# Kernel optimization log

Hardware: AMD Instinct MI355X
Metric: run time of the kernel (lower is better)

Reference implementation:

```python
import jax, jax.numpy as jnp
import numpy as np

N, E, B = 50000, 1600000, 64
VOCAB, EMB = 1000, 16
HID, OUT_FEAT = 192, 128   # hidden_sf*model_dim, out_sf*output_channels
MODEL_DIM, DEMO, OUT_DIM = 64, 5, 2
EPS = 1e-7  # GENConv eps


def setup_inputs() -> dict:
    key = jax.random.key(0)
    ks = jax.random.split(key, 18)
    f32 = jnp.float32

    def rn(k, shape, scale):
        return jax.random.normal(k, shape, dtype=f32) * scale

    node_idx = jax.random.randint(ks[0], (N,), 0, VOCAB)
    edge_index = jax.random.randint(ks[1], (2, E), 0, N)
    batch = jnp.sort(jax.random.randint(ks[2], (N,), 0, B))
    demographics = rn(ks[3], (B, DEMO), 1.0)

    emb = rn(ks[4], (VOCAB, EMB), 1.0)
    dims = [(EMB, HID), (HID, HID), (HID, HID), (HID, OUT_FEAT)]
    params = {}
    for i, (din, dout) in enumerate(dims):
        params[f"W{i}"] = rn(ks[5 + 2 * i], (din, dout), 1.0 / np.sqrt(din))
        params[f"b{i}"] = jnp.zeros((dout,), f32)
    params["Wc1"] = rn(ks[13], (OUT_FEAT + DEMO, MODEL_DIM), 1.0 / np.sqrt(OUT_FEAT + DEMO))
    params["bc1"] = jnp.zeros((MODEL_DIM,), f32)
    params["Wc2"] = rn(ks[14], (MODEL_DIM, OUT_DIM), 1.0 / np.sqrt(MODEL_DIM))
    params["bc2"] = jnp.zeros((OUT_DIM,), f32)

    return {"node_idx": node_idx, "edge_index": edge_index, "batch": batch,
            "demographics": demographics, "emb": emb, **params}


def _gen_conv(x, src, dst, W, b):
    # GENConv (num_layers=1, aggr='add', edge_attr=None):
    #   out_i = Linear( sum_{j->i} (relu(x_j) + eps) + x_i )
    m = jax.nn.relu(x) + EPS                                   # [N, D]
    agg = jax.ops.segment_sum(m[src], dst, num_segments=x.shape[0])
    return (agg + x) @ W + b


def reference(node_idx, edge_index, batch, demographics, emb,
              W0, b0, W1, b1, W2, b2, W3, b3, Wc1, bc1, Wc2, bc2):
    x = emb[node_idx]                                          # [N, 16]
    src, dst = edge_index[0], edge_index[1]
    for W, b in ((W0, b0), (W1, b1), (W2, b2), (W3, b3)):
        x = _gen_conv(x, src, dst, W, b)                       # [N, D_l]
    # global_mean_pool
    cnt = jax.ops.segment_sum(jnp.ones((x.shape[0],), x.dtype), batch, num_segments=B)
    g = jax.ops.segment_sum(x, batch, num_segments=B) / jnp.maximum(cnt, 1.0)[:, None]
    feats = jnp.concatenate([g, demographics], axis=1)         # [B, 133]
    h = jax.nn.relu(feats @ Wc1 + bc1)                         # dropout = identity (eval)
    return h @ Wc2 + bc2                                       # [B, out_dim]
```

## Files before the change

### kernel.cpp

```cpp
#include <hip/hip_runtime.h>
#include <stdint.h>

#define EPS 1e-7f

constexpr int N_NODES = 50000;
constexpr int N_EDGES = 1600000;
constexpr int BATCH = 64;
constexpr int EMB = 16;
constexpr int HID = 192;
constexpr int OUTF = 128;
constexpr int DEMO = 5;
constexpr int MODEL_DIM = 64;
constexpr int OUT_DIM = 2;

constexpr int NPART = 8;
constexpr int PART_NODES = (N_NODES + NPART - 1) / NPART;

constexpr int SCAN_CHUNK = 256;
constexpr int NCHUNK = (N_NODES + SCAN_CHUNK - 1) / SCAN_CHUNK;

typedef unsigned short bf16_t;
typedef short s8v __attribute__((ext_vector_type(8)));
typedef float f4v __attribute__((ext_vector_type(4)));

static __device__ __forceinline__ float bf2f(bf16_t u) {
  return __uint_as_float(((uint32_t)u) << 16);
}
static __device__ __forceinline__ bf16_t f2bf(float f) {
  uint32_t b = __float_as_uint(f);
  return (bf16_t)((b + 0x7FFFu + ((b >> 16) & 1u)) >> 16);
}

__global__ void emb_gather(const int* __restrict__ idx, const float* __restrict__ emb,
                           bf16_t* __restrict__ x) {
  int t = blockIdx.x * blockDim.x + threadIdx.x;
  if (t >= N_NODES * EMB) return;
  int node = t / EMB, f = t % EMB;
  x[t] = f2bf(emb[idx[node] * EMB + f]);
}

__global__ void hist_kernel(const int* __restrict__ dst, int* __restrict__ deg) {
  int part = blockIdx.x & (NPART - 1);
  int blk = blockIdx.x >> 3;
  int nthread = (gridDim.x >> 3) * blockDim.x;
  int lo = part * PART_NODES, hi = lo + PART_NODES;
  for (int e = blk * blockDim.x + threadIdx.x; e < N_EDGES; e += nthread) {
    int d = dst[e];
    if (d >= lo && d < hi) atomicAdd(&deg[d], 1);
  }
}

__global__ void chunk_sum_kernel(const int* __restrict__ deg, int* __restrict__ chunk_sum) {
  int i = blockIdx.x * SCAN_CHUNK + threadIdx.x;
  int v = (i < N_NODES) ? deg[i] : 0;
#pragma unroll
  for (int off = 32; off > 0; off >>= 1) v += __shfl_down(v, off);
  __shared__ int s[SCAN_CHUNK / 64];
  if ((threadIdx.x & 63) == 0) s[threadIdx.x >> 6] = v;
  __syncthreads();
  if (threadIdx.x == 0) {
    int t = 0;
#pragma unroll
    for (int w = 0; w < SCAN_CHUNK / 64; ++w) t += s[w];
    chunk_sum[blockIdx.x] = t;
  }
}

__global__ void scan_chunks_kernel(const int* __restrict__ chunk_sum,
                                   int* __restrict__ chunk_off) {
  __shared__ int s[256];
  int t = threadIdx.x;
  int v = (t < NCHUNK) ? chunk_sum[t] : 0;
  s[t] = v;
  __syncthreads();
  for (int off = 1; off < 256; off <<= 1) {
    int u = (t >= off) ? s[t - off] : 0;
    __syncthreads();
    s[t] += u;
    __syncthreads();
  }
  if (t < NCHUNK) chunk_off[t] = s[t] - v;
}

__global__ void chunk_scan_write_kernel(const int* __restrict__ deg,
                                        const int* __restrict__ chunk_off,
                                        int* __restrict__ row_start,
                                        int* __restrict__ cursor) {
  __shared__ int s[SCAN_CHUNK];
  int t = threadIdx.x;
  int i = blockIdx.x * SCAN_CHUNK + t;
  int v = (i < N_NODES) ? deg[i] : 0;
  s[t] = v;
  __syncthreads();
  for (int off = 1; off < SCAN_CHUNK; off <<= 1) {
    int u = (t >= off) ? s[t - off] : 0;
    __syncthreads();
    s[t] += u;
    __syncthreads();
  }
  int excl = chunk_off[blockIdx.x] + s[t] - v;
  if (i < N_NODES) {
    row_start[i] = excl;
    cursor[i] = excl;
    if (i == N_NODES - 1) row_start[N_NODES] = excl + v;
  }
}

__global__ void scatter_kernel(const int* __restrict__ src, const int* __restrict__ dst,
                               int* __restrict__ cursor, int* __restrict__ csr_src) {
  int part = blockIdx.x & (NPART - 1);
  int blk = blockIdx.x >> 3;
  int nthread = (gridDim.x >> 3) * blockDim.x;
  int lo = part * PART_NODES, hi = lo + PART_NODES;
  for (int e = blk * blockDim.x + threadIdx.x; e < N_EDGES; e += nthread) {
    int d = dst[e];
    if (d >= lo && d < hi) {
      int pos = atomicAdd(&cursor[d], 1);
      csr_src[pos] = src[e];
    }
  }
}

template <int TPN, int NPB>
__global__ void agg2_kernel(const uint32_t* __restrict__ x, const int* __restrict__ row_start,
                            const int* __restrict__ csr_src, uint32_t* __restrict__ out) {
  int f = threadIdx.x % TPN;
  int node = blockIdx.x * NPB + threadIdx.x / TPN;
  if (node >= N_NODES) return;
  int s0 = row_start[node], s1 = row_start[node + 1];
  float deps = (float)(s1 - s0) * EPS;
  uint32_t xv = x[(size_t)node * TPN + f];
  float a0 = __uint_as_float(xv << 16) + deps;
  float a1 = __uint_as_float(xv & 0xFFFF0000u) + deps;
  int e = s0;
  for (; e + 8 <= s1; e += 8) {
    int idx[8];
#pragma unroll
    for (int j = 0; j < 8; ++j) idx[j] = csr_src[e + j];
    uint32_t v[8];
#pragma unroll
    for (int j = 0; j < 8; ++j) v[j] = x[(size_t)idx[j] * TPN + f];
#pragma unroll
    for (int j = 0; j < 8; ++j) {
      a0 += fmaxf(__uint_as_float(v[j] << 16), 0.f);
      a1 += fmaxf(__uint_as_float(v[j] & 0xFFFF0000u), 0.f);
    }
  }
  for (; e < s1; ++e) {
    uint32_t v = x[(size_t)csr_src[e] * TPN + f];
    a0 += fmaxf(__uint_as_float(v << 16), 0.f);
    a1 += fmaxf(__uint_as_float(v & 0xFFFF0000u), 0.f);
  }
  out[(size_t)node * TPN + f] = (uint32_t)f2bf(a0) | ((uint32_t)f2bf(a1) << 16);
}

__global__ void wprep_kernel(const float* __restrict__ W, int K, int NOUT,
                             bf16_t* __restrict__ Wt) {
  int t = blockIdx.x * blockDim.x + threadIdx.x;
  if (t >= K * NOUT) return;
  int k = t / NOUT, n = t % NOUT;
  Wt[(size_t)n * K + k] = f2bf(W[t]);
}

template <int NOUT, bool OUT_BF16>
__global__ void mfma_gemm(const bf16_t* __restrict__ in, const bf16_t* __restrict__ Wt,
                          const float* __restrict__ bias, void* __restrict__ outp) {
  constexpr int K = 192;
  constexpr int KT = K / 32;
  constexpr int NT = NOUT / 16;
  int wave = threadIdx.x >> 6;
  int lane = threadIdx.x & 63;
  int tile = blockIdx.x * 4 + wave;
  if (tile >= N_NODES / 16) return;

  int rlo = lane & 15;
  int kbase = (lane >> 4) * 8;

  s8v a[KT];
  const bf16_t* ap = in + ((size_t)(tile * 16 + rlo)) * K + kbase;
#pragma unroll
  for (int kt = 0; kt < KT; ++kt) a[kt] = *(const s8v*)(ap + kt * 32);

  int r0 = (lane >> 4) * 4;
#pragma unroll
  for (int nt = 0; nt < NT; ++nt) {
    const bf16_t* wp = Wt + ((size_t)(nt * 16 + rlo)) * K + kbase;
    f4v c = {0.f, 0.f, 0.f, 0.f};
#pragma unroll
    for (int kt = 0; kt < KT; ++kt) {
      s8v b = *(const s8v*)(wp + kt * 32);
      c = __builtin_amdgcn_mfma_f32_16x16x32_bf16(a[kt], b, c, 0, 0, 0);
    }
    float bv = bias[nt * 16 + rlo];
#pragma unroll
    for (int r = 0; r < 4; ++r) {
      float v = c[r] + bv;
      size_t o = (size_t)(tile * 16 + r0 + r) * NOUT + nt * 16 + rlo;
      if constexpr (OUT_BF16) ((bf16_t*)outp)[o] = f2bf(v);
      else                    ((float*)outp)[o] = v;
    }
  }
}

template <int DIN, int DOUT, bool OUT_BF16>
__global__ void gemm_kernel(const bf16_t* __restrict__ in, const float* __restrict__ W,
                            const float* __restrict__ bias, void* __restrict__ outp) {
  constexpr int ROWS = 16;
  __shared__ bf16_t tile[ROWS * DIN];
  int c = threadIdx.x;
  int base = blockIdx.x * ROWS;

  {
    const uint4* gsrc = reinterpret_cast<const uint4*>(in + (size_t)base * DIN);
    uint4* ldst = reinterpret_cast<uint4*>(tile);
    constexpr int NV = ROWS * DIN * 2 / 16;
    for (int i = threadIdx.x; i < NV; i += blockDim.x) ldst[i] = gsrc[i];
  }
  __syncthreads();

  float acc[ROWS];
  float bc = bias[c];
#pragma unroll
  for (int r = 0; r < ROWS; ++r) acc[r] = bc;

  for (int k0 = 0; k0 < DIN; k0 += 8) {
    float w[8];
#pragma unroll
    for (int j = 0; j < 8; ++j) w[j] = W[(size_t)(k0 + j) * DOUT + c];
#pragma unroll
    for (int r = 0; r < ROWS; ++r) {
      uint4 packed = *reinterpret_cast<const uint4*>(&tile[r * DIN + k0]);
      uint32_t pk[4] = {packed.x, packed.y, packed.z, packed.w};
#pragma unroll
      for (int q = 0; q < 4; ++q) {
        float lo = __uint_as_float(pk[q] << 16);
        float hi = __uint_as_float(pk[q] & 0xFFFF0000u);
        acc[r] = fmaf(lo, w[2 * q], acc[r]);
        acc[r] = fmaf(hi, w[2 * q + 1], acc[r]);
      }
    }
  }

#pragma unroll
  for (int r = 0; r < ROWS; ++r) {
    size_t o = (size_t)(base + r) * DOUT + c;
    if constexpr (OUT_BF16) ((bf16_t*)outp)[o] = f2bf(acc[r]);
    else                    ((float*)outp)[o] = acc[r];
  }
}

constexpr int POOL_CHUNK = 100;
__global__ void pool_kernel(const float* __restrict__ x, const int* __restrict__ batch,
                            float* __restrict__ gsum, int* __restrict__ gcnt) {
  int f = threadIdx.x;
  int start = blockIdx.x * POOL_CHUNK;
  if (start >= N_NODES) return;
  int end = min(start + POOL_CHUNK, N_NODES);
  int cur = batch[start];
  float acc = 0.f;
  int cnt = 0;
  for (int i = start; i < end; ++i) {
    int b = batch[i];
    if (b != cur) {
      atomicAdd(&gsum[cur * OUTF + f], acc);
      if (f == 0) atomicAdd(&gcnt[cur], cnt);
      acc = 0.f; cnt = 0; cur = b;
    }
    acc += x[(size_t)i * OUTF + f];
    cnt++;
  }
  atomicAdd(&gsum[cur * OUTF + f], acc);
  if (f == 0) atomicAdd(&gcnt[cur], cnt);
}

__global__ void mlp_kernel(const float* __restrict__ gsum, const int* __restrict__ gcnt,
                           const float* __restrict__ demo,
                           const float* __restrict__ Wc1, const float* __restrict__ bc1,
                           const float* __restrict__ Wc2, const float* __restrict__ bc2,
                           float* __restrict__ out) {
  int b = blockIdx.x;
  int c = threadIdx.x;
  __shared__ float feats[OUTF + DEMO];
  float inv = 1.f / fmaxf((float)gcnt[b], 1.f);
  for (int k = c; k < OUTF; k += MODEL_DIM) feats[k] = gsum[b * OUTF + k] * inv;
  if (c < DEMO) feats[OUTF + c] = demo[b * DEMO + c];
  __syncthreads();
  float s = bc1[c];
#pragma unroll
  for (int k = 0; k < OUTF + DEMO; ++k) s = fmaf(feats[k], Wc1[k * MODEL_DIM + c], s);
  float h = fmaxf(s, 0.f);
  float o0 = h * Wc2[c * OUT_DIM + 0];
  float o1 = h * Wc2[c * OUT_DIM + 1];
#pragma unroll
  for (int off = 32; off > 0; off >>= 1) {
    o0 += __shfl_down(o0, off);
    o1 += __shfl_down(o1, off);
  }
  if (c == 0) {
    out[b * OUT_DIM + 0] = o0 + bc2[0];
    out[b * OUT_DIM + 1] = o1 + bc2[1];
  }
}

extern "C" void kernel_launch(void* const* d_in, const int* in_sizes, int n_in,
                              void* d_out, int out_size, void* d_ws, size_t ws_size,
                              hipStream_t stream) {
  const int*   node_idx = (const int*)d_in[0];
  const int*   edge_index = (const int*)d_in[1];
  const int*   batch = (const int*)d_in[2];
  const float* demo = (const float*)d_in[3];
  const float* emb  = (const float*)d_in[4];
  const float* W0 = (const float*)d_in[5];  const float* b0 = (const float*)d_in[6];
  const float* W1 = (const float*)d_in[7];  const float* b1 = (const float*)d_in[8];
  const float* W2 = (const float*)d_in[9];  const float* b2 = (const float*)d_in[10];
  const float* W3 = (const float*)d_in[11]; const float* b3 = (const float*)d_in[12];
  const float* Wc1 = (const float*)d_in[13]; const float* bc1 = (const float*)d_in[14];
  const float* Wc2 = (const float*)d_in[15]; const float* bc2 = (const float*)d_in[16];
  const int* src = edge_index;
  const int* dst = edge_index + N_EDGES;
  float* out = (float*)d_out;

  char* ws = (char*)d_ws;
  size_t off = 0;
  auto alloc = [&](size_t bytes) {
    void* p = ws + off;
    off += (bytes + 255) & ~size_t(255);
    return p;
  };
  bf16_t* xbf     = (bf16_t*)alloc((size_t)N_NODES * HID * 2);
  bf16_t* aggbf   = (bf16_t*)alloc((size_t)N_NODES * HID * 2);
  float*  x3      = (float*)alloc((size_t)N_NODES * OUTF * 4);
  int*   csr_src  = (int*)alloc((size_t)N_EDGES * 4);
  int*   deg      = (int*)alloc((size_t)N_NODES * 4);
  int*   row_start= (int*)alloc((size_t)(N_NODES + 1) * 4);
  int*   cursor   = (int*)alloc((size_t)N_NODES * 4);
  int*   chunk_sum= (int*)alloc((size_t)NCHUNK * 4);
  int*   chunk_off= (int*)alloc((size_t)NCHUNK * 4);
  float* gsum     = (float*)alloc((size_t)BATCH * OUTF * 4);
  int*   gcnt     = (int*)alloc((size_t)BATCH * 4);
  bf16_t* Wt1     = (bf16_t*)alloc((size_t)HID * HID * 2);
  bf16_t* Wt2     = (bf16_t*)alloc((size_t)HID * HID * 2);
  bf16_t* Wt3     = (bf16_t*)alloc((size_t)OUTF * HID * 2);

  hipMemsetAsync(deg, 0, (size_t)N_NODES * 4, stream);
  hipMemsetAsync(gsum, 0, (size_t)BATCH * OUTF * 4, stream);
  hipMemsetAsync(gcnt, 0, (size_t)BATCH * 4, stream);

  wprep_kernel<<<(HID * HID + 255) / 256, 256, 0, stream>>>(W1, HID, HID, Wt1);
  wprep_kernel<<<(HID * HID + 255) / 256, 256, 0, stream>>>(W2, HID, HID, Wt2);
  wprep_kernel<<<(HID * OUTF + 255) / 256, 256, 0, stream>>>(W3, HID, OUTF, Wt3);

  hist_kernel<<<NPART * 256, 256, 0, stream>>>(dst, deg);
  chunk_sum_kernel<<<NCHUNK, SCAN_CHUNK, 0, stream>>>(deg, chunk_sum);
  scan_chunks_kernel<<<1, 256, 0, stream>>>(chunk_sum, chunk_off);
  chunk_scan_write_kernel<<<NCHUNK, SCAN_CHUNK, 0, stream>>>(deg, chunk_off, row_start, cursor);
  scatter_kernel<<<NPART * 256, 256, 0, stream>>>(src, dst, cursor, csr_src);

  constexpr int TILES = N_NODES / 16;
  constexpr int GBLK = (TILES + 3) / 4;

  emb_gather<<<(N_NODES * EMB + 255) / 256, 256, 0, stream>>>(node_idx, emb, xbf);
  agg2_kernel<8, 32><<<(N_NODES + 31) / 32, 256, 0, stream>>>(
      (const uint32_t*)xbf, row_start, csr_src, (uint32_t*)aggbf);
  gemm_kernel<16, 192, true><<<N_NODES / 16, 192, 0, stream>>>(aggbf, W0, b0, xbf);
  agg2_kernel<96, 2><<<(N_NODES + 1) / 2, 192, 0, stream>>>(
      (const uint32_t*)xbf, row_start, csr_src, (uint32_t*)aggbf);
  mfma_gemm<192, true><<<GBLK, 256, 0, stream>>>(aggbf, Wt1, b1, xbf);
  agg2_kernel<96, 2><<<(N_NODES + 1) / 2, 192, 0, stream>>>(
      (const uint32_t*)xbf, row_start, csr_src, (uint32_t*)aggbf);
  mfma_gemm<192, true><<<GBLK, 256, 0, stream>>>(aggbf, Wt2, b2, xbf);
  agg2_kernel<96, 2><<<(N_NODES + 1) / 2, 192, 0, stream>>>(
      (const uint32_t*)xbf, row_start, csr_src, (uint32_t*)aggbf);
  mfma_gemm<128, false><<<GBLK, 256, 0, stream>>>(aggbf, Wt3, b3, x3);

  pool_kernel<<<(N_NODES + POOL_CHUNK - 1) / POOL_CHUNK, OUTF, 0, stream>>>(x3, batch, gsum, gcnt);
  mlp_kernel<<<BATCH, MODEL_DIM, 0, stream>>>(gsum, gcnt, demo, Wc1, bc1, Wc2, bc2, out);
}
```

Measured before the change: 588.3 us.

## Split hidden-layer aggregation into feature-column slices across blocks

Replaces the per-node full-row gather aggregation for the 192-wide layers with a sliced kernel. Each block handles 16 nodes and only one eighth of the feature columns (12 packed bf16 pairs). Consecutive block IDs map to different slices, aiming to improve cache locality for the randomly gathered source rows, since each slice's working set is smaller. In exchange, neighbour indices are re-read once per slice and each gather touches only 48 bytes per row, which may lower memory coalescing efficiency.

```diff
diff --git a/kernel.cpp b/kernel.cpp
--- a/kernel.cpp
+++ b/kernel.cpp
@@ -152,6 +152,47 @@
     a1 += fmaxf(__uint_as_float(v & 0xFFFF0000u), 0.f);
   }
   out[(size_t)node * TPN + f] = (uint32_t)f2bf(a0) | ((uint32_t)f2bf(a1) << 16);
+}
+
+constexpr int SL_TPN = 12;
+constexpr int SL_NPB = 16;
+__global__ void agg2_slice_kernel(const uint32_t* __restrict__ x,
+                                  const int* __restrict__ row_start,
+                                  const int* __restrict__ csr_src,
+                                  uint32_t* __restrict__ out) {
+  constexpr int ROW = HID / 2;
+  int slice = blockIdx.x & (NPART - 1);
+  int grp = blockIdx.x >> 3;
+  int f = threadIdx.x % SL_TPN;
+  int node = grp * SL_NPB + threadIdx.x / SL_TPN;
+  if (node >= N_NODES) return;
+  int col = slice * SL_TPN + f;
+  int s0 = row_start[node], s1 = row_start[node + 1];
+  float deps = (float)(s1 - s0) * EPS;
+  const uint32_t* xc = x + col;
+  uint32_t xv = xc[(size_t)node * ROW];
+  float a0 = __uint_as_float(xv << 16) + deps;
+  float a1 = __uint_as_float(xv & 0xFFFF0000u) + deps;
+  int e = s0;
+  for (; e + 8 <= s1; e += 8) {
+    int idx[8];
+#pragma unroll
+    for (int j = 0; j < 8; ++j) idx[j] = csr_src[e + j];
+    uint32_t v[8];
+#pragma unroll
+    for (int j = 0; j < 8; ++j) v[j] = xc[(size_t)idx[j] * ROW];
+#pragma unroll
+    for (int j = 0; j < 8; ++j) {
+      a0 += fmaxf(__uint_as_float(v[j] << 16), 0.f);
+      a1 += fmaxf(__uint_as_float(v[j] & 0xFFFF0000u), 0.f);
+    }
+  }
+  for (; e < s1; ++e) {
+    uint32_t v = xc[(size_t)csr_src[e] * ROW];
+    a0 += fmaxf(__uint_as_float(v << 16), 0.f);
+    a1 += fmaxf(__uint_as_float(v & 0xFFFF0000u), 0.f);
+  }
+  out[(size_t)node * ROW + col] = (uint32_t)f2bf(a0) | ((uint32_t)f2bf(a1) << 16);
 }
 
 __global__ void wprep_kernel(const float* __restrict__ W, int K, int NOUT,
@@ -358,18 +399,19 @@
 
   constexpr int TILES = N_NODES / 16;
   constexpr int GBLK = (TILES + 3) / 4;
+  constexpr int SL_GRID = NPART * ((N_NODES + SL_NPB - 1) / SL_NPB);
 
   emb_gather<<<(N_NODES * EMB + 255) / 256, 256, 0, stream>>>(node_idx, emb, xbf);
   agg2_kernel<8, 32><<<(N_NODES + 31) / 32, 256, 0, stream>>>(
       (const uint32_t*)xbf, row_start, csr_src, (uint32_t*)aggbf);
   gemm_kernel<16, 192, true><<<N_NODES / 16, 192, 0, stream>>>(aggbf, W0, b0, xbf);
-  agg2_kernel<96, 2><<<(N_NODES + 1) / 2, 192, 0, stream>>>(
+  agg2_slice_kernel<<<SL_GRID, SL_TPN * SL_NPB, 0, stream>>>(
       (const uint32_t*)xbf, row_start, csr_src, (uint32_t*)aggbf);
   mfma_gemm<192, true><<<GBLK, 256, 0, stream>>>(aggbf, Wt1, b1, xbf);
-  agg2_kernel<96, 2><<<(N_NODES + 1) / 2, 192, 0, stream>>>(
+  agg2_slice_kernel<<<SL_GRID, SL_TPN * SL_NPB, 0, stream>>>(
       (const uint32_t*)xbf, row_start, csr_src, (uint32_t*)aggbf);
   mfma_gemm<192, true><<<GBLK, 256, 0, stream>>>(aggbf, Wt2, b2, xbf);
-  agg2_kernel<96, 2><<<(N_NODES + 1) / 2, 192, 0, stream>>>(
+  agg2_slice_kernel<<<SL_GRID, SL_TPN * SL_NPB, 0, stream>>>(
       (const uint32_t*)xbf, row_start, csr_src, (uint32_t*)aggbf);
   mfma_gemm<128, false><<<GBLK, 256, 0, stream>>>(aggbf, Wt3, b3, x3);
 
```

After: 1.121 ms. +90.6%, slower.

## Bucket CSR neighbors by source range and vectorize 192-wide aggregation

Applied to the files above, without the earlier changes.

CSR construction now counts edges per (destination, source bucket) pair, with 16 buckets, and scans that larger histogram. Within each row, neighbor indices end up grouped by source-node range, which is meant to improve L2 locality of the gathers during aggregation. The 192-wide aggregation layers also switch to a new kernel in which each thread loads 16-byte uint4 vectors (8 bf16 features), giving fewer, wider memory requests per neighbor. The cost is a 16x larger histogram with its memset, a longer scan, and more scattered atomics during CSR build.

```diff
diff --git a/kernel.cpp b/kernel.cpp
--- a/kernel.cpp
+++ b/kernel.cpp
@@ -16,8 +16,12 @@
 constexpr int NPART = 8;
 constexpr int PART_NODES = (N_NODES + NPART - 1) / NPART;
 
-constexpr int SCAN_CHUNK = 256;
-constexpr int NCHUNK = (N_NODES + SCAN_CHUNK - 1) / SCAN_CHUNK;
+constexpr int NBKT = 16;
+constexpr int BKT_DIV = (N_NODES + NBKT - 1) / NBKT;
+constexpr int NB2 = N_NODES * NBKT;
+
+constexpr int SCAN2_CHUNK = 1024;
+constexpr int NCHUNK2 = (NB2 + SCAN2_CHUNK - 1) / SCAN2_CHUNK;
 
 typedef unsigned short bf16_t;
 typedef short s8v __attribute__((ext_vector_type(8)));
@@ -39,39 +43,67 @@
   x[t] = f2bf(emb[idx[node] * EMB + f]);
 }
 
-__global__ void hist_kernel(const int* __restrict__ dst, int* __restrict__ deg) {
+__global__ void hist2_kernel(const int* __restrict__ src, const int* __restrict__ dst,
+                             int* __restrict__ hist2) {
   int part = blockIdx.x & (NPART - 1);
   int blk = blockIdx.x >> 3;
   int nthread = (gridDim.x >> 3) * blockDim.x;
   int lo = part * PART_NODES, hi = lo + PART_NODES;
   for (int e = blk * blockDim.x + threadIdx.x; e < N_EDGES; e += nthread) {
     int d = dst[e];
-    if (d >= lo && d < hi) atomicAdd(&deg[d], 1);
-  }
-}
-
-__global__ void chunk_sum_kernel(const int* __restrict__ deg, int* __restrict__ chunk_sum) {
-  int i = blockIdx.x * SCAN_CHUNK + threadIdx.x;
-  int v = (i < N_NODES) ? deg[i] : 0;
+    if (d >= lo && d < hi) atomicAdd(&hist2[d * NBKT + src[e] / BKT_DIV], 1);
+  }
+}
+
+__global__ void chunk_sum2_kernel(const int* __restrict__ hist2, int* __restrict__ chunk_sum) {
+  int t = threadIdx.x;
+  int base = blockIdx.x * SCAN2_CHUNK + t * 4;
+  int v = 0;
+#pragma unroll
+  for (int j = 0; j < 4; ++j) {
+    int i = base + j;
+    if (i < NB2) v += hist2[i];
+  }
 #pragma unroll
   for (int off = 32; off > 0; off >>= 1) v += __shfl_down(v, off);
-  __shared__ int s[SCAN_CHUNK / 64];
-  if ((threadIdx.x & 63) == 0) s[threadIdx.x >> 6] = v;
+  __shared__ int s[4];
+  if ((t & 63) == 0) s[t >> 6] = v;
   __syncthreads();
-  if (threadIdx.x == 0) {
-    int t = 0;
-#pragma unroll
-    for (int w = 0; w < SCAN_CHUNK / 64; ++w) t += s[w];
-    chunk_sum[blockIdx.x] = t;
-  }
-}
-
-__global__ void scan_chunks_kernel(const int* __restrict__ chunk_sum,
-                                   int* __restrict__ chunk_off) {
+  if (t == 0) chunk_sum[blockIdx.x] = s[0] + s[1] + s[2] + s[3];
+}
+
+__global__ void scan_chunks2_kernel(const int* __restrict__ chunk_sum,
+                                    int* __restrict__ chunk_off) {
+  __shared__ int s[1024];
+  int t = threadIdx.x;
+  int v = (t < NCHUNK2) ? chunk_sum[t] : 0;
+  s[t] = v;
+  __syncthreads();
+  for (int off = 1; off < 1024; off <<= 1) {
+    int u = (t >= off) ? s[t - off] : 0;
+    __syncthreads();
+    s[t] += u;
+    __syncthreads();
+  }
+  if (t < NCHUNK2) chunk_off[t] = s[t] - v;
+}
+
+__global__ void chunk_scan_write2_kernel(const int* __restrict__ hist2,
+                                         const int* __restrict__ chunk_off,
+                                         int* __restrict__ cursor2,
+                                         int* __restrict__ row_start) {
   __shared__ int s[256];
   int t = threadIdx.x;
-  int v = (t < NCHUNK) ? chunk_sum[t] : 0;
-  s[t] = v;
+  int base = blockIdx.x * SCAN2_CHUNK + t * 4;
+  int local[4];
+  int tsum = 0;
+#pragma unroll
+  for (int j = 0; j < 4; ++j) {
+    int i = base + j;
+    local[j] = (i < NB2) ? hist2[i] : 0;
+    tsum += local[j];
+  }
+  s[t] = tsum;
   __syncthreads();
   for (int off = 1; off < 256; off <<= 1) {
     int u = (t >= off) ? s[t - off] : 0;
@@ -79,35 +111,21 @@
     s[t] += u;
     __syncthreads();
   }
-  if (t < NCHUNK) chunk_off[t] = s[t] - v;
-}
-
-__global__ void chunk_scan_write_kernel(const int* __restrict__ deg,
-                                        const int* __restrict__ chunk_off,
-                                        int* __restrict__ row_start,
-                                        int* __restrict__ cursor) {
-  __shared__ int s[SCAN_CHUNK];
-  int t = threadIdx.x;
-  int i = blockIdx.x * SCAN_CHUNK + t;
-  int v = (i < N_NODES) ? deg[i] : 0;
-  s[t] = v;
-  __syncthreads();
-  for (int off = 1; off < SCAN_CHUNK; off <<= 1) {
-    int u = (t >= off) ? s[t - off] : 0;
-    __syncthreads();
-    s[t] += u;
-    __syncthreads();
-  }
-  int excl = chunk_off[blockIdx.x] + s[t] - v;
-  if (i < N_NODES) {
-    row_start[i] = excl;
-    cursor[i] = excl;
-    if (i == N_NODES - 1) row_start[N_NODES] = excl + v;
+  int run = chunk_off[blockIdx.x] + s[t] - tsum;
+#pragma unroll
+  for (int j = 0; j < 4; ++j) {
+    int i = base + j;
+    if (i < NB2) {
+      cursor2[i] = run;
+      if ((i & (NBKT - 1)) == 0) row_start[i / NBKT] = run;
+      if (i == NB2 - 1) row_start[N_NODES] = run + local[j];
+      run += local[j];
+    }
   }
 }
 
 __global__ void scatter_kernel(const int* __restrict__ src, const int* __restrict__ dst,
-                               int* __restrict__ cursor, int* __restrict__ csr_src) {
+                               int* __restrict__ cursor2, int* __restrict__ csr_src) {
   int part = blockIdx.x & (NPART - 1);
   int blk = blockIdx.x >> 3;
   int nthread = (gridDim.x >> 3) * blockDim.x;
@@ -115,8 +133,9 @@
   for (int e = blk * blockDim.x + threadIdx.x; e < N_EDGES; e += nthread) {
     int d = dst[e];
     if (d >= lo && d < hi) {
-      int pos = atomicAdd(&cursor[d], 1);
-      csr_src[pos] = src[e];
+      int s = src[e];
+      int pos = atomicAdd(&cursor2[d * NBKT + s / BKT_DIV], 1);
+      csr_src[pos] = s;
     }
   }
 }
@@ -152,6 +171,61 @@
     a1 += fmaxf(__uint_as_float(v & 0xFFFF0000u), 0.f);
   }
   out[(size_t)node * TPN + f] = (uint32_t)f2bf(a0) | ((uint32_t)f2bf(a1) << 16);
+}
+
+constexpr int A4_TPN = 24;
+constexpr int A4_NPB = 8;
+__global__ void agg4_kernel(const uint4* __restrict__ x, const int* __restrict__ row_start,
+                            const int* __restrict__ csr_src, uint4* __restrict__ out) {
+  constexpr int ROW = 24;
+  int f = threadIdx.x % A4_TPN;
+  int node = blockIdx.x * A4_NPB + threadIdx.x / A4_TPN;
+  if (node >= N_NODES) return;
+  int s0 = row_start[node], s1 = row_start[node + 1];
+  float deps = (float)(s1 - s0) * EPS;
+  uint4 xv = x[(size_t)node * ROW + f];
+  float a[8];
+  {
+    uint32_t pk[4] = {xv.x, xv.y, xv.z, xv.w};
+#pragma unroll
+    for (int q = 0; q < 4; ++q) {
+      a[2 * q]     = __uint_as_float(pk[q] << 16) + deps;
+      a[2 * q + 1] = __uint_as_float(pk[q] & 0xFFFF0000u) + deps;
+    }
+  }
+  int e = s0;
+  for (; e + 4 <= s1; e += 4) {
+    int idx[4];
+#pragma unroll
+    for (int j = 0; j < 4; ++j) idx[j] = csr_src[e + j];
+    uint4 v[4];
+#pragma unroll
+    for (int j = 0; j < 4; ++j) v[j] = x[(size_t)idx[j] * ROW + f];
+#pragma unroll
+    for (int j = 0; j < 4; ++j) {
+      uint32_t pk[4] = {v[j].x, v[j].y, v[j].z, v[j].w};
+#pragma unroll
+      for (int q = 0; q < 4; ++q) {
+        a[2 * q]     += fmaxf(__uint_as_float(pk[q] << 16), 0.f);
+        a[2 * q + 1] += fmaxf(__uint_as_float(pk[q] & 0xFFFF0000u), 0.f);
+      }
+    }
+  }
+  for (; e < s1; ++e) {
+    uint4 v = x[(size_t)csr_src[e] * ROW + f];
+    uint32_t pk[4] = {v.x, v.y, v.z, v.w};
+#pragma unroll
+    for (int q = 0; q < 4; ++q) {
+      a[2 * q]     += fmaxf(__uint_as_float(pk[q] << 16), 0.f);
+      a[2 * q + 1] += fmaxf(__uint_as_float(pk[q] & 0xFFFF0000u), 0.f);
+    }
+  }
+  uint4 o;
+  o.x = (uint32_t)f2bf(a[0]) | ((uint32_t)f2bf(a[1]) << 16);
+  o.y = (uint32_t)f2bf(a[2]) | ((uint32_t)f2bf(a[3]) << 16);
+  o.z = (uint32_t)f2bf(a[4]) | ((uint32_t)f2bf(a[5]) << 16);
+  o.w = (uint32_t)f2bf(a[6]) | ((uint32_t)f2bf(a[7]) << 16);
+  out[(size_t)node * ROW + f] = o;
 }
 
 __global__ void wprep_kernel(const float* __restrict__ W, int K, int NOUT,
@@ -331,18 +405,18 @@
   bf16_t* aggbf   = (bf16_t*)alloc((size_t)N_NODES * HID * 2);
   float*  x3      = (float*)alloc((size_t)N_NODES * OUTF * 4);
   int*   csr_src  = (int*)alloc((size_t)N_EDGES * 4);
-  int*   deg      = (int*)alloc((size_t)N_NODES * 4);
+  int*   hist2    = (int*)alloc((size_t)NB2 * 4);
+  int*   cursor2  = (int*)alloc((size_t)NB2 * 4);
   int*   row_start= (int*)alloc((size_t)(N_NODES + 1) * 4);
-  int*   cursor   = (int*)alloc((size_t)N_NODES * 4);
-  int*   chunk_sum= (int*)alloc((size_t)NCHUNK * 4);
-  int*   chunk_off= (int*)alloc((size_t)NCHUNK * 4);
+  int*   chunk_sum= (int*)alloc((size_t)NCHUNK2 * 4);
+  int*   chunk_off= (int*)alloc((size_t)NCHUNK2 * 4);
   float* gsum     = (float*)alloc((size_t)BATCH * OUTF * 4);
   int*   gcnt     = (int*)alloc((size_t)BATCH * 4);
   bf16_t* Wt1     = (bf16_t*)alloc((size_t)HID * HID * 2);
   bf16_t* Wt2     = (bf16_t*)alloc((size_t)HID * HID * 2);
   bf16_t* Wt3     = (bf16_t*)alloc((size_t)OUTF * HID * 2);
 
-  hipMemsetAsync(deg, 0, (size_t)N_NODES * 4, stream);
+  hipMemsetAsync(hist2, 0, (size_t)NB2 * 4, stream);
   hipMemsetAsync(gsum, 0, (size_t)BATCH * OUTF * 4, stream);
   hipMemsetAsync(gcnt, 0, (size_t)BATCH * 4, stream);
 
@@ -350,27 +424,28 @@
   wprep_kernel<<<(HID * HID + 255) / 256, 256, 0, stream>>>(W2, HID, HID, Wt2);
   wprep_kernel<<<(HID * OUTF + 255) / 256, 256, 0, stream>>>(W3, HID, OUTF, Wt3);
 
-  hist_kernel<<<NPART * 256, 256, 0, stream>>>(dst, deg);
-  chunk_sum_kernel<<<NCHUNK, SCAN_CHUNK, 0, stream>>>(deg, chunk_sum);
-  scan_chunks_kernel<<<1, 256, 0, stream>>>(chunk_sum, chunk_off);
-  chunk_scan_write_kernel<<<NCHUNK, SCAN_CHUNK, 0, stream>>>(deg, chunk_off, row_start, cursor);
-  scatter_kernel<<<NPART * 256, 256, 0, stream>>>(src, dst, cursor, csr_src);
+  hist2_kernel<<<NPART * 256, 256, 0, stream>>>(src, dst, hist2);
+  chunk_sum2_kernel<<<NCHUNK2, 256, 0, stream>>>(hist2, chunk_sum);
+  scan_chunks2_kernel<<<1, 1024, 0, stream>>>(chunk_sum, chunk_off);
+  chunk_scan_write2_kernel<<<NCHUNK2, 256, 0, stream>>>(hist2, chunk_off, cursor2, row_start);
+  scatter_kernel<<<NPART * 256, 256, 0, stream>>>(src, dst, cursor2, csr_src);
 
   constexpr int TILES = N_NODES / 16;
   constexpr int GBLK = (TILES + 3) / 4;
+  constexpr int A4_GRID = (N_NODES + A4_NPB - 1) / A4_NPB;
 
   emb_gather<<<(N_NODES * EMB + 255) / 256, 256, 0, stream>>>(node_idx, emb, xbf);
   agg2_kernel<8, 32><<<(N_NODES + 31) / 32, 256, 0, stream>>>(
       (const uint32_t*)xbf, row_start, csr_src, (uint32_t*)aggbf);
   gemm_kernel<16, 192, true><<<N_NODES / 16, 192, 0, stream>>>(aggbf, W0, b0, xbf);
-  agg2_kernel<96, 2><<<(N_NODES + 1) / 2, 192, 0, stream>>>(
-      (const uint32_t*)xbf, row_start, csr_src, (uint32_t*)aggbf);
+  agg4_kernel<<<A4_GRID, A4_TPN * A4_NPB, 0, stream>>>(
+      (const uint4*)xbf, row_start, csr_src, (uint4*)aggbf);
   mfma_gemm<192, true><<<GBLK, 256, 0, stream>>>(aggbf, Wt1, b1, xbf);
-  agg2_kernel<96, 2><<<(N_NODES + 1) / 2, 192, 0, stream>>>(
-      (const uint32_t*)xbf, row_start, csr_src, (uint32_t*)aggbf);
+  agg4_kernel<<<A4_GRID, A4_TPN * A4_NPB, 0, stream>>>(
+      (const uint4*)xbf, row_start, csr_src, (uint4*)aggbf);
   mfma_gemm<192, true><<<GBLK, 256, 0, stream>>>(aggbf, Wt2, b2, xbf);
-  agg2_kernel<96, 2><<<(N_NODES + 1) / 2, 192, 0, stream>>>(
-      (const uint32_t*)xbf, row_start, csr_src, (uint32_t*)aggbf);
+  agg4_kernel<<<A4_GRID, A4_TPN * A4_NPB, 0, stream>>>(
+      (const uint4*)xbf, row_start, csr_src, (uint4*)aggbf);
   mfma_gemm<128, false><<<GBLK, 256, 0, stream>>>(aggbf, Wt3, b3, x3);
 
   pool_kernel<<<(N_NODES + POOL_CHUNK - 1) / POOL_CHUNK, OUTF, 0, stream>>>(x3, batch, gsum, gcnt);
```

After: 557.9 us. 1.05x faster.

## Store hidden features in 32-column slices for cache-local neighbor aggregation

Applied to the files above, without the earlier changes.

The GEMM epilogues now write hidden activations in a slice-major layout: six slices of 32 bf16 columns, each slice contiguous across all nodes. A new aggregation kernel assigns each slice to its own blocks (blockIdx low bits), and each thread gathers 16-byte chunks. The goal is for one slice of the gathered table (about 3.2 MB) to stay in L2/MALL while random neighbor reads hit it, instead of touching the full 19 MB row-major table. The trade-offs are strided scattered stores in the GEMM epilogue, two of eight block slots per group doing no work, and more index reads because every slice re-reads the CSR lists.

```diff
diff --git a/kernel.cpp b/kernel.cpp
--- a/kernel.cpp
+++ b/kernel.cpp
@@ -15,6 +15,9 @@
 
 constexpr int NPART = 8;
 constexpr int PART_NODES = (N_NODES + NPART - 1) / NPART;
+
+constexpr int NSLICE = 6;
+constexpr int SLICE_U4 = 4;
 
 constexpr int SCAN_CHUNK = 256;
 constexpr int NCHUNK = (N_NODES + SCAN_CHUNK - 1) / SCAN_CHUNK;
@@ -154,6 +157,63 @@
   out[(size_t)node * TPN + f] = (uint32_t)f2bf(a0) | ((uint32_t)f2bf(a1) << 16);
 }
 
+constexpr int AS_NPB = 64;
+__global__ void agg_slice_kernel(const uint4* __restrict__ xs, const int* __restrict__ row_start,
+                                 const int* __restrict__ csr_src, uint4* __restrict__ out) {
+  int s = blockIdx.x & (NPART - 1);
+  if (s >= NSLICE) return;
+  int grp = blockIdx.x >> 3;
+  int f = threadIdx.x & 3;
+  int node = grp * AS_NPB + (threadIdx.x >> 2);
+  if (node >= N_NODES) return;
+  int s0 = row_start[node], s1 = row_start[node + 1];
+  float deps = (float)(s1 - s0) * EPS;
+  const uint4* base = xs + (size_t)s * N_NODES * SLICE_U4 + f;
+  uint4 xv = base[(size_t)node * SLICE_U4];
+  float a[8];
+  {
+    uint32_t pk[4] = {xv.x, xv.y, xv.z, xv.w};
+#pragma unroll
+    for (int q = 0; q < 4; ++q) {
+      a[2 * q]     = __uint_as_float(pk[q] << 16) + deps;
+      a[2 * q + 1] = __uint_as_float(pk[q] & 0xFFFF0000u) + deps;
+    }
+  }
+  int e = s0;
+  for (; e + 8 <= s1; e += 8) {
+    int idx[8];
+#pragma unroll
+    for (int j = 0; j < 8; ++j) idx[j] = csr_src[e + j];
+    uint4 v[8];
+#pragma unroll
+    for (int j = 0; j < 8; ++j) v[j] = base[(size_t)idx[j] * SLICE_U4];
+#pragma unroll
+    for (int j = 0; j < 8; ++j) {
+      uint32_t pk[4] = {v[j].x, v[j].y, v[j].z, v[j].w};
+#pragma unroll
+      for (int q = 0; q < 4; ++q) {
+        a[2 * q]     += fmaxf(__uint_as_float(pk[q] << 16), 0.f);
+        a[2 * q + 1] += fmaxf(__uint_as_float(pk[q] & 0xFFFF0000u), 0.f);
+      }
+    }
+  }
+  for (; e < s1; ++e) {
+    uint4 v = base[(size_t)csr_src[e] * SLICE_U4];
+    uint32_t pk[4] = {v.x, v.y, v.z, v.w};
+#pragma unroll
+    for (int q = 0; q < 4; ++q) {
+      a[2 * q]     += fmaxf(__uint_as_float(pk[q] << 16), 0.f);
+      a[2 * q + 1] += fmaxf(__uint_as_float(pk[q] & 0xFFFF0000u), 0.f);
+    }
+  }
+  uint4 o;
+  o.x = (uint32_t)f2bf(a[0]) | ((uint32_t)f2bf(a[1]) << 16);
+  o.y = (uint32_t)f2bf(a[2]) | ((uint32_t)f2bf(a[3]) << 16);
+  o.z = (uint32_t)f2bf(a[4]) | ((uint32_t)f2bf(a[5]) << 16);
+  o.w = (uint32_t)f2bf(a[6]) | ((uint32_t)f2bf(a[7]) << 16);
+  out[(size_t)node * (HID / 8) + s * SLICE_U4 + f] = o;
+}
+
 __global__ void wprep_kernel(const float* __restrict__ W, int K, int NOUT,
                              bf16_t* __restrict__ Wt) {
   int t = blockIdx.x * blockDim.x + threadIdx.x;
@@ -162,7 +222,7 @@
   Wt[(size_t)n * K + k] = f2bf(W[t]);
 }
 
-template <int NOUT, bool OUT_BF16>
+template <int NOUT, bool OUT_BF16, bool SLICED>
 __global__ void mfma_gemm(const bf16_t* __restrict__ in, const bf16_t* __restrict__ Wt,
                           const float* __restrict__ bias, void* __restrict__ outp) {
   constexpr int K = 192;
@@ -191,20 +251,27 @@
       s8v b = *(const s8v*)(wp + kt * 32);
       c = __builtin_amdgcn_mfma_f32_16x16x32_bf16(a[kt], b, c, 0, 0, 0);
     }
-    float bv = bias[nt * 16 + rlo];
+    int col = nt * 16 + rlo;
+    float bv = bias[col];
 #pragma unroll
     for (int r = 0; r < 4; ++r) {
       float v = c[r] + bv;
-      size_t o = (size_t)(tile * 16 + r0 + r) * NOUT + nt * 16 + rlo;
-      if constexpr (OUT_BF16) ((bf16_t*)outp)[o] = f2bf(v);
-      else                    ((float*)outp)[o] = v;
-    }
-  }
-}
-
-template <int DIN, int DOUT, bool OUT_BF16>
-__global__ void gemm_kernel(const bf16_t* __restrict__ in, const float* __restrict__ W,
-                            const float* __restrict__ bias, void* __restrict__ outp) {
+      int row = tile * 16 + r0 + r;
+      if constexpr (SLICED) {
+        int sl = col >> 5, w = col & 31;
+        ((bf16_t*)outp)[((size_t)(sl * N_NODES + row)) * 32 + w] = f2bf(v);
+      } else {
+        size_t o = (size_t)row * NOUT + col;
+        if constexpr (OUT_BF16) ((bf16_t*)outp)[o] = f2bf(v);
+        else                    ((float*)outp)[o] = v;
+      }
+    }
+  }
+}
+
+template <int DIN, int DOUT>
+__global__ void gemm_sliced_kernel(const bf16_t* __restrict__ in, const float* __restrict__ W,
+                                   const float* __restrict__ bias, bf16_t* __restrict__ outp) {
   constexpr int ROWS = 16;
   __shared__ bf16_t tile[ROWS * DIN];
   int c = threadIdx.x;
@@ -241,12 +308,10 @@
     }
   }
 
-#pragma unroll
-  for (int r = 0; r < ROWS; ++r) {
-    size_t o = (size_t)(base + r) * DOUT + c;
-    if constexpr (OUT_BF16) ((bf16_t*)outp)[o] = f2bf(acc[r]);
-    else                    ((float*)outp)[o] = acc[r];
-  }
+  int sl = c >> 5, w = c & 31;
+#pragma unroll
+  for (int r = 0; r < ROWS; ++r)
+    outp[((size_t)(sl * N_NODES + base + r)) * 32 + w] = f2bf(acc[r]);
 }
 
 constexpr int POOL_CHUNK = 100;
@@ -327,8 +392,9 @@
     off += (bytes + 255) & ~size_t(255);
     return p;
   };
-  bf16_t* xbf     = (bf16_t*)alloc((size_t)N_NODES * HID * 2);
+  bf16_t* xsl     = (bf16_t*)alloc((size_t)NSLICE * N_NODES * 32 * 2);
   bf16_t* aggbf   = (bf16_t*)alloc((size_t)N_NODES * HID * 2);
+  bf16_t* xbf0    = (bf16_t*)alloc((size_t)N_NODES * EMB * 2);
   float*  x3      = (float*)alloc((size_t)N_NODES * OUTF * 4);
   int*   csr_src  = (int*)alloc((size_t)N_EDGES * 4);
   int*   deg      = (int*)alloc((size_t)N_NODES * 4);
@@ -358,20 +424,21 @@
 
   constexpr int TILES = N_NODES / 16;
   constexpr int GBLK = (TILES + 3) / 4;
-
-  emb_gather<<<(N_NODES * EMB + 255) / 256, 256, 0, stream>>>(node_idx, emb, xbf);
+  constexpr int AS_GRID = NPART * ((N_NODES + AS_NPB - 1) / AS_NPB);
+
+  emb_gather<<<(N_NODES * EMB + 255) / 256, 256, 0, stream>>>(node_idx, emb, xbf0);
   agg2_kernel<8, 32><<<(N_NODES + 31) / 32, 256, 0, stream>>>(
-      (const uint32_t*)xbf, row_start, csr_src, (uint32_t*)aggbf);
-  gemm_kernel<16, 192, true><<<N_NODES / 16, 192, 0, stream>>>(aggbf, W0, b0, xbf);
-  agg2_kernel<96, 2><<<(N_NODES + 1) / 2, 192, 0, stream>>>(
-      (const uint32_t*)xbf, row_start, csr_src, (uint32_t*)aggbf);
-  mfma_gemm<192, true><<<GBLK, 256, 0, stream>>>(aggbf, Wt1, b1, xbf);
-  agg2_kernel<96, 2><<<(N_NODES + 1) / 2, 192, 0, stream>>>(
-      (const uint32_t*)xbf, row_start, csr_src, (uint32_t*)aggbf);
-  mfma_gemm<192, true><<<GBLK, 256, 0, stream>>>(aggbf, Wt2, b2, xbf);
-  agg2_kernel<96, 2><<<(N_NODES + 1) / 2, 192, 0, stream>>>(
-      (const uint32_t*)xbf, row_start, csr_src, (uint32_t*)aggbf);
-  mfma_gemm<128, false><<<GBLK, 256, 0, stream>>>(aggbf, Wt3, b3, x3);
+      (const uint32_t*)xbf0, row_start, csr_src, (uint32_t*)aggbf);
+  gemm_sliced_kernel<16, 192><<<N_NODES / 16, 192, 0, stream>>>(aggbf, W0, b0, xsl);
+  agg_slice_kernel<<<AS_GRID, 256, 0, stream>>>(
+      (const uint4*)xsl, row_start, csr_src, (uint4*)aggbf);
+  mfma_gemm<192, true, true><<<GBLK, 256, 0, stream>>>(aggbf, Wt1, b1, xsl);
+  agg_slice_kernel<<<AS_GRID, 256, 0, stream>>>(
+      (const uint4*)xsl, row_start, csr_src, (uint4*)aggbf);
+  mfma_gemm<192, true, true><<<GBLK, 256, 0, stream>>>(aggbf, Wt2, b2, xsl);
+  agg_slice_kernel<<<AS_GRID, 256, 0, stream>>>(
+      (const uint4*)xsl, row_start, csr_src, (uint4*)aggbf);
+  mfma_gemm<128, false, false><<<GBLK, 256, 0, stream>>>(aggbf, Wt3, b3, x3);
 
   pool_kernel<<<(N_NODES + POOL_CHUNK - 1) / POOL_CHUNK, OUTF, 0, stream>>>(x3, batch, gsum, gcnt);
   mlp_kernel<<<BATCH, MODEL_DIM, 0, stream>>>(gsum, gcnt, demo, Wc1, bc1, Wc2, bc2, out);
```

Measured after the change: 626.7 us. +6.5%, slower.
